# Optimization experiments

Measured on AMD Instinct MI355X. Metric: run time of the kernel, lower is better.

## Reference

```python
import jax, jax.numpy as jnp
import numpy as np

B, C, H, W = 128, 256, 32, 32
TD, NHEADS, PH, PW = 192, 4, 4, 4
FF = 384
MAXG = 8
TABLE = (2 * MAXG - 1) ** 2  # 225


def setup_inputs() -> dict:
    key = jax.random.key(0)
    ks = jax.random.split(key, 10)
    rn = lambda k, shape, s=0.02: jax.random.normal(k, shape, jnp.float32) * s
    return {
        "x": jax.random.normal(ks[0], (B, C, H, W), jnp.float32),
        "conv1_w": rn(ks[1], (TD, C)),          # 1x1 conv, no bias
        "conv2_w": rn(ks[2], (C, TD)),          # 1x1 conv, no bias
        "qkv_w": rn(ks[3], (TD, 3 * TD)), "qkv_b": jnp.zeros((3 * TD,), jnp.float32),
        "proj_w": rn(ks[4], (TD, TD)), "proj_b": jnp.zeros((TD,), jnp.float32),
        "ffn_w1": rn(ks[5], (TD, FF)), "ffn_b1": jnp.zeros((FF,), jnp.float32),
        "ffn_w2": rn(ks[6], (FF, TD)), "ffn_b2": jnp.zeros((TD,), jnp.float32),
        "ln1_g": jnp.ones((TD,), jnp.float32), "ln1_b": jnp.zeros((TD,), jnp.float32),
        "ln2_g": jnp.ones((TD,), jnp.float32), "ln2_b": jnp.zeros((TD,), jnp.float32),
        "alpha": rn(ks[7], (1,), 0.1),
        "rpb_table": rn(ks[8], (TABLE, NHEADS)),
    }


def _ln(x, g, b, eps=1e-5):
    m = x.mean(-1, keepdims=True)
    v = ((x - m) ** 2).mean(-1, keepdims=True)
    return (x - m) * jax.lax.rsqrt(v + eps) * g + b


def _rpb_index(Nh, Nw, maxg):
    # static (trace-time) relative position index over the patch grid
    ch, cw = np.meshgrid(np.arange(Nh), np.arange(Nw), indexing="ij")
    coords = np.stack([ch.ravel(), cw.ravel()])                 # (2, N)
    rel = coords[:, :, None] - coords[:, None, :]               # (2, N, N)
    idx = (rel[0] + maxg - 1) * (2 * maxg - 1) + (rel[1] + maxg - 1)
    return jnp.asarray(idx.reshape(-1), jnp.int32)              # (N*N,)


def reference(x, conv1_w, conv2_w, qkv_w, qkv_b, proj_w, proj_b,
              ffn_w1, ffn_b1, ffn_w2, ffn_b2,
              ln1_g, ln1_b, ln2_g, ln2_b, alpha, rpb_table):
    Nh, Nw = H // PH, W // PW
    Np = Nh * Nw
    hd = TD // NHEADS
    scale = 1.0 / np.sqrt(hd).astype(np.float32)

    # local 1x1 conv
    xl = jnp.einsum("bchw,tc->bthw", x, conv1_w)                # (B, TD, H, W)
    # patchify + mean-pool -> one token per patch
    xp = xl.reshape(B, TD, Nh, PH, Nw, PW).transpose(0, 2, 4, 3, 5, 1)
    xp = xp.reshape(B, Np, PH * PW, TD)
    tokens = xp.mean(axis=2)                                    # (B, Np, TD)

    # attention with gathered relative position bias
    t = _ln(tokens, ln1_g, ln1_b)
    qkv = (t @ qkv_w + qkv_b).reshape(B, Np, 3, NHEADS, hd)
    q, k, v = qkv[:, :, 0], qkv[:, :, 1], qkv[:, :, 2]          # (B, Np, H, hd)
    attn = jnp.einsum("bnhd,bmhd->bhnm", q, k) * scale
    bias = rpb_table[_rpb_index(Nh, Nw, MAXG)]                  # (Np*Np, heads)
    bias = bias.reshape(Np, Np, NHEADS).transpose(2, 0, 1)      # (heads, Np, Np)
    attn = jax.nn.softmax(attn + bias[None], axis=-1)
    o = jnp.einsum("bhnm,bmhd->bnhd", attn, v).reshape(B, Np, TD)
    o = o @ proj_w + proj_b

    out = tokens + alpha * o                                    # scaled residual
    h2 = _ln(out, ln2_g, ln2_b)
    out = out + (jax.nn.gelu(h2 @ ffn_w1 + ffn_b1, approximate=False) @ ffn_w2 + ffn_b2)

    # unpatchify: broadcast each token back over its ph*pw pixels
    ot = jnp.broadcast_to(out[:, :, None, :], (B, Np, PH * PW, TD))
    ot = ot.reshape(B, Nh, Nw, PH, PW, TD).transpose(0, 5, 1, 3, 2, 4)
    ot = ot.reshape(B, TD, H, W)
    return x + jnp.einsum("bthw,ct->bchw", ot, conv2_w)
```

## Files before the change

kernel.cpp:

```cpp
#include <hip/hip_runtime.h>
#include <hip/hip_bf16.h>

#define Bsz 128
#define Cch 256
#define Him 32
#define Wim 32
#define TD 192
#define NH 4
#define HD 48
#define FF 384
#define NP 64

typedef float f32x4 __attribute__((ext_vector_type(4)));
typedef __bf16 bf16x8 __attribute__((ext_vector_type(8)));
typedef unsigned int u32;

#define MFMA(a, b, c) __builtin_amdgcn_mfma_f32_16x16x32_bf16(a, b, c, 0, 0, 0)
#define LD8(p) (*reinterpret_cast<const bf16x8*>(p))
#define VM0 asm volatile("s_waitcnt vmcnt(0)" ::: "memory")
#define VM2 asm volatile("s_waitcnt vmcnt(2)" ::: "memory")
#define VMB do { if (wlow) { asm volatile("s_waitcnt vmcnt(4)" ::: "memory"); } \
                 else      { asm volatile("s_waitcnt vmcnt(2)" ::: "memory"); } } while (0)
#define LGKM0 asm volatile("s_waitcnt lgkmcnt(0)" ::: "memory")
#define SBAR __builtin_amdgcn_s_barrier()

__device__ __forceinline__ ushort f2bf(float f) {
    union { __hip_bfloat16 h; ushort u; } cv;
    cv.h = __float2bfloat16(f);
    return cv.u;
}

__device__ __forceinline__ void gload16(const void* g, void* l) {
    __builtin_amdgcn_global_load_lds((const __attribute__((address_space(1))) u32*)g,
                                     (__attribute__((address_space(3))) u32*)l, 16, 0, 0);
}

template <int K2B>
__device__ __forceinline__ void stageW(char* lbuf, const char* g0, int colStrB, int tid) {
    constexpr int CHB = 32 * K2B;
    constexpr int NR = (CHB + 8191) / 8192;
#pragma unroll
    for (int rd = 0; rd < NR; ++rd) {
        int p = rd * 8192 + tid * 16;
        if (p < CHB) {
            int col = p / K2B;
            int kb = (p - col * K2B) ^ ((col & 7) << 4);
            gload16(g0 + (size_t)col * colStrB + kb, lbuf + p);
        }
    }
}

typedef ushort ushort8v __attribute__((ext_vector_type(8)));
__global__ __launch_bounds__(256) void prep_kernel(const float* __restrict__ x,
                                                   const float* __restrict__ c1,
                                                   const float* __restrict__ c2,
                                                   const float* __restrict__ qw,
                                                   const float* __restrict__ pw,
                                                   const float* __restrict__ f1,
                                                   const float* __restrict__ f2,
                                                   ushort* __restrict__ wb,
                                                   ushort* __restrict__ xm) {
    const int bb = blockIdx.x;
    const int tid = threadIdx.x;
    if (bb < 1536) {
        int g = bb * 256 + tid;
        float v;
        if (g < 49152) v = c1[g];
        else if (g < 98304) v = c2[g - 49152];
        else if (g < 208896) { int i = g - 98304;  int n = i / 192, k = i - n * 192; v = qw[k * 576 + n]; }
        else if (g < 245760) { int i = g - 208896; int n = i / 192, k = i - n * 192; v = pw[k * 192 + n]; }
        else if (g < 319488) { int i = g - 245760; int n = i / 192, k = i - n * 192; v = f1[k * 384 + n]; }
        else                 { int i = g - 319488; int n = i / 384, k = i - n * 384; v = f2[k * 192 + n]; }
        wb[g] = f2bf(v);
        return;
    }
    __shared__ float acc[32][65];
    int pb = bb - 1536;
    int b = pb >> 3, cg = pb & 7;
    int c = tid >> 3, wq = tid & 7;
    const float* pl = x + ((size_t)(b * Cch + cg * 32 + c) * 1024) + wq * 4;
#pragma unroll 1
    for (int nh = 0; nh < 8; ++nh) {
        const float* p0 = pl + nh * 128;
        float4 v0 = *reinterpret_cast<const float4*>(p0);
        float4 v1 = *reinterpret_cast<const float4*>(p0 + 32);
        float4 v2 = *reinterpret_cast<const float4*>(p0 + 64);
        float4 v3 = *reinterpret_cast<const float4*>(p0 + 96);
        float s = v0.x + v0.y + v0.z + v0.w + v1.x + v1.y + v1.z + v1.w +
                  v2.x + v2.y + v2.z + v2.w + v3.x + v3.y + v3.z + v3.w;
        acc[c][nh * 8 + wq] = s * 0.0625f;
    }
    __syncthreads();
    int p = tid >> 2, c8 = (tid & 3) * 8;
    ushort8v o;
#pragma unroll
    for (int k = 0; k < 8; ++k) o[k] = f2bf(acc[c8 + k][p]);
    *reinterpret_cast<ushort8v*>(xm + ((size_t)(b * 64 + p)) * 256 + cg * 32 + c8) = o;
}

__global__ __launch_bounds__(512, 1) void token_kernel(
    const ushort* __restrict__ xm, const ushort* __restrict__ wb,
    const float* __restrict__ qkv_b, const float* __restrict__ proj_b,
    const float* __restrict__ ffn_b1, const float* __restrict__ ffn_b2,
    const float* __restrict__ ln1_g, const float* __restrict__ ln1_b,
    const float* __restrict__ ln2_g, const float* __restrict__ ln2_b,
    const float* __restrict__ alphap, const float* __restrict__ rpb,
    ushort* __restrict__ y) {
    __shared__ __align__(16) char LDS[154624];
    ushort* tln = (ushort*)(LDS);
    ushort* qb  = (ushort*)(LDS + 25600);
    ushort* kb  = (ushort*)(LDS + 51200);
    ushort* vT  = (ushort*)(LDS + 76800);
    char*   SBB = LDS + 104448;
    float2* scr2 = (float2*)(LDS + 153600);
    ushort* t2  = tln;
    ushort* obp = qb;
    ushort* h0  = qb;
    ushort* h1  = kb;
    ushort* o2  = vT;
#define SBUF(i) (SBB + (i) * 12288)

    const int b = blockIdx.x;
    const int tid = threadIdx.x, lane = tid & 63, w = tid >> 6;
    const int l15 = lane & 15, slot = lane >> 4, slot16 = slot * 16;
    const int r = w >> 1, cc = w & 1;
    const int rowA = r * 16 + l15;
    const int orow = r * 16 + slot * 4;
    const int xp = (l15 & 7) << 4;
    const int colB = cc * 16 + l15;
    const bool wlow = (w < 4);

    float qbr[18], f1br[12], l1gr[6], l1br[6], l2gr[6], l2br[6], pbr[6], f2br[6];
#pragma unroll
    for (int j = 0; j < 18; ++j) qbr[j] = qkv_b[(j / 6) * 192 + (j % 6) * 32 + colB];
#pragma unroll
    for (int j = 0; j < 12; ++j) f1br[j] = ffn_b1[j * 32 + colB];
#pragma unroll
    for (int c = 0; c < 6; ++c) {
        int col = c * 32 + colB;
        l1gr[c] = ln1_g[col]; l1br[c] = ln1_b[col];
        l2gr[c] = ln2_g[col]; l2br[c] = ln2_b[col];
        pbr[c] = proj_b[col]; f2br[c] = ffn_b2[col];
    }
    const float alpha = alphap[0];

    const char* xrow = (const char*)xm + ((size_t)(b * 64 + rowA)) * 512;
    bf16x8 a1[2][4];
#pragma unroll
    for (int kh = 0; kh < 2; ++kh)
#pragma unroll
        for (int ks = 0; ks < 4; ++ks)
            a1[kh][ks] = LD8(xrow + kh * 256 + ks * 64 + slot16);

    const char* c1g = (const char*)wb;
    const char* qg  = (const char*)(wb + 98304);
    const char* pg  = (const char*)(wb + 208896);
    const char* fg  = (const char*)(wb + 245760);
    const char* f2g = (const char*)(wb + 319488);
    const char* c2g = (const char*)(wb + 49152);

    f32x4 tok[6], pj[6];
#pragma unroll
    for (int c = 0; c < 6; ++c) { tok[c] = f32x4{0,0,0,0}; pj[c] = f32x4{0,0,0,0}; }

    stageW<256>(SBUF(0), c1g, 512, tid);
    stageW<256>(SBUF(1), c1g + 256, 512, tid);
    stageW<256>(SBUF(2), c1g + 16384, 512, tid);
#pragma unroll
    for (int j = 0; j < 12; ++j) {
        if (j < 10) VM2; else VM0;
        SBAR;
        if (j < 9) {
            int jn = j + 3;
            stageW<256>(SBUF(jn & 3), c1g + (size_t)(jn >> 1) * 16384 + (jn & 1) * 256, 512, tid);
        }
        const char* bp = SBUF(j & 3) + colB * 256;
        int c = j >> 1, kh = j & 1;
#pragma unroll
        for (int ks = 0; ks < 4; ++ks)
            tok[c] = MFMA(a1[kh][ks], LD8(bp + ((ks * 64 + slot16) ^ xp)), tok[c]);
    }
    stageW<384>(SBUF(0), qg, 384, tid);
    stageW<384>(SBUF(1), qg + 12288, 384, tid);
    stageW<384>(SBUF(2), qg + 24576, 384, tid);
    {
        float s[4] = {}, s2[4] = {};
#pragma unroll
        for (int c = 0; c < 6; ++c)
#pragma unroll
            for (int j2 = 0; j2 < 4; ++j2) { float v = tok[c][j2]; s[j2] += v; s2[j2] += v * v; }
#pragma unroll
        for (int m = 1; m < 16; m <<= 1)
#pragma unroll
            for (int j2 = 0; j2 < 4; ++j2) { s[j2] += __shfl_xor(s[j2], m); s2[j2] += __shfl_xor(s2[j2], m); }
        if (l15 == 0)
#pragma unroll
            for (int j2 = 0; j2 < 4; ++j2) scr2[(orow + j2) * 2 + cc] = make_float2(s[j2], s2[j2]);
        LGKM0; SBAR;
#pragma unroll
        for (int j2 = 0; j2 < 4; ++j2) {
            int row = orow + j2;
            float2 eA = scr2[row * 2], eB = scr2[row * 2 + 1];
            float mean = (eA.x + eB.x) * (1.f / 192.f);
            float inv = rsqrtf((eA.y + eB.y) * (1.f / 192.f) - mean * mean + 1e-5f);
#pragma unroll
            for (int c = 0; c < 6; ++c)
                tln[row * 200 + c * 32 + colB] = f2bf((tok[c][j2] - mean) * inv * l1gr[c] + l1br[c]);
        }
        LGKM0; SBAR;
    }

    {
        bf16x8 aT[6];
        const char* trow = (const char*)tln + rowA * 400;
#pragma unroll
        for (int ks = 0; ks < 6; ++ks) aT[ks] = LD8(trow + ks * 64 + slot16);
#pragma unroll
        for (int j = 0; j < 18; ++j) {
            if (j < 16) VMB; else VM0;
            SBAR;
            if (j < 15) stageW<384>(SBUF((j + 3) & 3), qg + (size_t)(j + 3) * 12288, 384, tid);
            const char* bp = SBUF(j & 3) + colB * 384;
            f32x4 acc = f32x4{0,0,0,0};
#pragma unroll
            for (int ks = 0; ks < 6; ++ks)
                acc = MFMA(aT[ks], LD8(bp + ((ks * 64 + slot16) ^ xp)), acc);
            int col = (j % 6) * 32 + colB;
            float bias = qbr[j];
            if (j < 6) {
#pragma unroll
                for (int j2 = 0; j2 < 4; ++j2) qb[(orow + j2) * 200 + col] = f2bf(acc[j2] + bias);
            } else if (j < 12) {
#pragma unroll
                for (int j2 = 0; j2 < 4; ++j2) kb[(orow + j2) * 200 + col] = f2bf(acc[j2] + bias);
            } else {
                ushort4 pk;
                pk.x = f2bf(acc[0] + bias); pk.y = f2bf(acc[1] + bias);
                pk.z = f2bf(acc[2] + bias); pk.w = f2bf(acc[3] + bias);
                *reinterpret_cast<ushort4*>(&vT[col * 72 + orow]) = pk;
            }
        }
    }
    LGKM0; SBAR;

    {
        const float scale = 0.14433756729740643f;
        ushort* P2b0 = (ushort*)(LDS + cc * 9216);
        ushort* P2b1 = (ushort*)(LDS + 104448 + cc * 9216);
#pragma unroll
        for (int p = 0; p < 2; ++p) {
            int h = p * 2 + cc;
            ushort* P2 = p ? P2b1 : P2b0;
            float rb[4][4];
#pragma unroll
            for (int j2 = 0; j2 < 4; ++j2) {
                int qrow = orow + j2, qh = qrow >> 3, qw = qrow & 7;
#pragma unroll
                for (int nf = 0; nf < 4; ++nf) {
                    int krow = l15 + nf * 16;
                    rb[j2][nf] = rpb[((qh - (krow >> 3) + 7) * 15 + (qw - (krow & 7) + 7)) * 4 + h];
                }
            }
            uint4 z = make_uint4(0, 0, 0, 0);
            const char* qrp = (const char*)qb + rowA * 400 + h * 96;
            uint4 qa1 = *(const uint4*)(qrp + slot16);
            uint4 qa2 = (slot < 2) ? *(const uint4*)(qrp + 64 + slot16) : z;
            f32x4 S[4] = {};
#pragma unroll
            for (int nf = 0; nf < 4; ++nf) {
                const char* kp = (const char*)kb + (l15 + nf * 16) * 400 + h * 96;
                uint4 k1 = *(const uint4*)(kp + slot16);
                uint4 k2 = (slot < 2) ? *(const uint4*)(kp + 64 + slot16) : z;
                S[nf] = MFMA(*(bf16x8*)&qa1, *(bf16x8*)&k1, S[nf]);
                S[nf] = MFMA(*(bf16x8*)&qa2, *(bf16x8*)&k2, S[nf]);
            }
#pragma unroll
            for (int j2 = 0; j2 < 4; ++j2) {
                float sv[4]; float mx = -1e30f;
#pragma unroll
                for (int nf = 0; nf < 4; ++nf) { sv[nf] = S[nf][j2] * scale + rb[j2][nf]; mx = fmaxf(mx, sv[nf]); }
#pragma unroll
                for (int m = 1; m < 16; m <<= 1) mx = fmaxf(mx, __shfl_xor(mx, m));
                float sum = 0.f;
#pragma unroll
                for (int nf = 0; nf < 4; ++nf) { sv[nf] = expf(sv[nf] - mx); sum += sv[nf]; }
#pragma unroll
                for (int m = 1; m < 16; m <<= 1) sum += __shfl_xor(sum, m);
                float inv = 1.f / sum;
                int qrow = orow + j2;
#pragma unroll
                for (int nf = 0; nf < 4; ++nf) P2[qrow * 72 + l15 + nf * 16] = f2bf(sv[nf] * inv);
            }
        }
        LGKM0; SBAR;
#pragma unroll
        for (int p = 0; p < 2; ++p) {
            int h = p * 2 + cc;
            ushort* P2 = p ? P2b1 : P2b0;
            f32x4 O[3] = {};
            const char* prow = (const char*)P2 + rowA * 144;
#pragma unroll
            for (int ki = 0; ki < 2; ++ki) {
                bf16x8 pa = LD8(prow + ki * 64 + slot16);
#pragma unroll
                for (int nf = 0; nf < 3; ++nf) {
                    bf16x8 vb = LD8((const char*)vT + (h * 48 + l15 + nf * 16) * 144 + ki * 64 + slot16);
                    O[nf] = MFMA(pa, vb, O[nf]);
                }
            }
#pragma unroll
            for (int nf = 0; nf < 3; ++nf)
#pragma unroll
                for (int j2 = 0; j2 < 4; ++j2)
                    obp[(orow + j2) * 200 + h * 48 + l15 + nf * 16] = f2bf(O[nf][j2]);
        }
        LGKM0; SBAR;
    }
    stageW<384>(SBUF(0), pg, 384, tid);
    stageW<384>(SBUF(1), pg + 12288, 384, tid);
    stageW<384>(SBUF(2), pg + 24576, 384, tid);

    {
        bf16x8 aO[6];
        const char* orw = (const char*)obp + rowA * 400;
#pragma unroll
        for (int ks = 0; ks < 6; ++ks) aO[ks] = LD8(orw + ks * 64 + slot16);
#pragma unroll
        for (int j = 0; j < 6; ++j) {
            if (j < 4) VMB; else VM0;
            SBAR;
            if (j < 3) stageW<384>(SBUF((j + 3) & 3), pg + (size_t)(j + 3) * 12288, 384, tid);
            const char* bp = SBUF(j & 3) + colB * 384;
#pragma unroll
            for (int ks = 0; ks < 6; ++ks)
                pj[j] = MFMA(aO[ks], LD8(bp + ((ks * 64 + slot16) ^ xp)), pj[j]);
        }
    }
    SBAR;
    stageW<384>(SBUF(0), fg, 384, tid);
    stageW<384>(SBUF(1), fg + 12288, 384, tid);
    stageW<384>(SBUF(2), fg + 24576, 384, tid);
    {
        float s[4] = {}, s2[4] = {};
#pragma unroll
        for (int c = 0; c < 6; ++c)
#pragma unroll
            for (int j2 = 0; j2 < 4; ++j2) {
                float v = tok[c][j2] + alpha * (pj[c][j2] + pbr[c]);
                pj[c][j2] = v;
                s[j2] += v; s2[j2] += v * v;
            }
#pragma unroll
        for (int m = 1; m < 16; m <<= 1)
#pragma unroll
            for (int j2 = 0; j2 < 4; ++j2) { s[j2] += __shfl_xor(s[j2], m); s2[j2] += __shfl_xor(s2[j2], m); }
        if (l15 == 0)
#pragma unroll
            for (int j2 = 0; j2 < 4; ++j2) scr2[(orow + j2) * 2 + cc] = make_float2(s[j2], s2[j2]);
        LGKM0; SBAR;
#pragma unroll
        for (int j2 = 0; j2 < 4; ++j2) {
            int row = orow + j2;
            float2 eA = scr2[row * 2], eB = scr2[row * 2 + 1];
            float mean = (eA.x + eB.x) * (1.f / 192.f);
            float inv = rsqrtf((eA.y + eB.y) * (1.f / 192.f) - mean * mean + 1e-5f);
#pragma unroll
            for (int c = 0; c < 6; ++c)
                t2[row * 200 + c * 32 + colB] = f2bf((pj[c][j2] - mean) * inv * l2gr[c] + l2br[c]);
        }
        LGKM0; SBAR;
    }

    {
        bf16x8 aT2[6];
        const char* trow = (const char*)t2 + rowA * 400;
#pragma unroll
        for (int ks = 0; ks < 6; ++ks) aT2[ks] = LD8(trow + ks * 64 + slot16);
#pragma unroll
        for (int j = 0; j < 12; ++j) {
            if (j < 10) VMB; else VM0;
            SBAR;
            if (j < 9) stageW<384>(SBUF((j + 3) & 3), fg + (size_t)(j + 3) * 12288, 384, tid);
            const char* bp = SBUF(j & 3) + colB * 384;
            f32x4 acc = f32x4{0,0,0,0};
#pragma unroll
            for (int ks = 0; ks < 6; ++ks)
                acc = MFMA(aT2[ks], LD8(bp + ((ks * 64 + slot16) ^ xp)), acc);
            int col384 = j * 32 + colB;
            ushort* hb = (j < 6) ? h0 : h1;
            int lcol = (j < 6) ? col384 : col384 - 192;
#pragma unroll
            for (int j2 = 0; j2 < 4; ++j2) {
                float v = acc[j2] + f1br[j];
                v = 0.5f * v * (1.f + erff(v * 0.70710678118654752f));
                hb[(orow + j2) * 200 + lcol] = f2bf(v);
            }
        }
    }
    LGKM0; SBAR;
    stageW<384>(SBUF(0), f2g, 768, tid);
    stageW<384>(SBUF(1), f2g + 384, 768, tid);
    stageW<384>(SBUF(2), f2g + 24576, 768, tid);

    f32x4 f2a[6];
#pragma unroll
    for (int c = 0; c < 6; ++c) f2a[c] = f32x4{0,0,0,0};
    {
        bf16x8 ah[2][6];
        const char* h0r = (const char*)h0 + rowA * 400;
        const char* h1r = (const char*)h1 + rowA * 400;
#pragma unroll
        for (int ks = 0; ks < 6; ++ks) {
            ah[0][ks] = LD8(h0r + ks * 64 + slot16);
            ah[1][ks] = LD8(h1r + ks * 64 + slot16);
        }
#pragma unroll
        for (int j = 0; j < 12; ++j) {
            if (j < 10) VMB; else VM0;
            SBAR;
            if (j < 9) {
                int jn = j + 3;
                stageW<384>(SBUF(jn & 3), f2g + (size_t)(jn >> 1) * 24576 + (jn & 1) * 384, 768, tid);
            }
            const char* bp = SBUF(j & 3) + colB * 384;
            int c = j >> 1, kh = j & 1;
#pragma unroll
            for (int ks = 0; ks < 6; ++ks)
                f2a[c] = MFMA(ah[kh][ks], LD8(bp + ((ks * 64 + slot16) ^ xp)), f2a[c]);
        }
    }
    stageW<384>(SBUF(0), c2g, 384, tid);
    stageW<384>(SBUF(1), c2g + 12288, 384, tid);
    stageW<384>(SBUF(2), c2g + 24576, 384, tid);
#pragma unroll
    for (int c = 0; c < 6; ++c) {
        int col = c * 32 + colB;
#pragma unroll
        for (int j2 = 0; j2 < 4; ++j2)
            o2[(orow + j2) * 200 + col] = f2bf(pj[c][j2] + f2a[c][j2] + f2br[c]);
    }
    LGKM0; SBAR;

    {
        bf16x8 aO2[6];
        const char* o2r = (const char*)o2 + rowA * 400;
#pragma unroll
        for (int ks = 0; ks < 6; ++ks) aO2[ks] = LD8(o2r + ks * 64 + slot16);
        ushort* yb = y + (size_t)b * 64 * 256;
#pragma unroll
        for (int j = 0; j < 8; ++j) {
            if (j < 6) VMB; else VM0;
            SBAR;
            if (j < 5) stageW<384>(SBUF((j + 3) & 3), c2g + (size_t)(j + 3) * 12288, 384, tid);
            const char* bp = SBUF(j & 3) + colB * 384;
            f32x4 acc = f32x4{0,0,0,0};
#pragma unroll
            for (int ks = 0; ks < 6; ++ks)
                acc = MFMA(aO2[ks], LD8(bp + ((ks * 64 + slot16) ^ xp)), acc);
            int col = j * 32 + colB;
#pragma unroll
            for (int j2 = 0; j2 < 4; ++j2)
                yb[(size_t)(orow + j2) * 256 + col] = f2bf(acc[j2]);
        }
    }
#undef SBUF
}

__global__ __launch_bounds__(256) void final_kernel(const float* __restrict__ x,
                                                    const ushort* __restrict__ y,
                                                    float* __restrict__ out) {
    size_t g = (size_t)blockIdx.x * 256 + threadIdx.x;
    int w4 = g & 7, hh = (g >> 3) & 31, c = (g >> 8) & 255, b = (int)(g >> 16);
    int p = (hh >> 2) * 8 + w4;
    u32 yu = y[((size_t)b * NP + p) * Cch + c];
    union { u32 u; float f; } cv; cv.u = yu << 16;
    float yv = cv.f;
    f32x4 xv = *(reinterpret_cast<const f32x4*>(x) + g);
    f32x4 ov = {xv.x + yv, xv.y + yv, xv.z + yv, xv.w + yv};
    __builtin_nontemporal_store(ov, reinterpret_cast<f32x4*>(out) + g);
}

extern "C" void kernel_launch(void* const* d_in, const int* in_sizes, int n_in,
                              void* d_out, int out_size, void* d_ws, size_t ws_size,
                              hipStream_t stream) {
    const float* x       = (const float*)d_in[0];
    const float* conv1_w = (const float*)d_in[1];
    const float* conv2_w = (const float*)d_in[2];
    const float* qkv_w   = (const float*)d_in[3];
    const float* qkv_b   = (const float*)d_in[4];
    const float* proj_w  = (const float*)d_in[5];
    const float* proj_b  = (const float*)d_in[6];
    const float* ffn_w1  = (const float*)d_in[7];
    const float* ffn_b1  = (const float*)d_in[8];
    const float* ffn_w2  = (const float*)d_in[9];
    const float* ffn_b2  = (const float*)d_in[10];
    const float* ln1_g   = (const float*)d_in[11];
    const float* ln1_b   = (const float*)d_in[12];
    const float* ln2_g   = (const float*)d_in[13];
    const float* ln2_b   = (const float*)d_in[14];
    const float* alpha   = (const float*)d_in[15];
    const float* rpb     = (const float*)d_in[16];
    float* out = (float*)d_out;

    ushort* ybuf = (ushort*)d_ws;
    ushort* xm   = ybuf + 2097152;
    ushort* wb   = xm + 2097152;

    prep_kernel<<<2560, 256, 0, stream>>>(x, conv1_w, conv2_w, qkv_w, proj_w, ffn_w1, ffn_w2,
                                          wb, xm);
    token_kernel<<<Bsz, 512, 0, stream>>>(xm, wb, qkv_b, proj_b, ffn_b1, ffn_b2,
                                          ln1_g, ln1_b, ln2_g, ln2_b, alpha, rpb, ybuf);
    final_kernel<<<(Bsz * Cch * Him * Wim) / 1024, 256, 0, stream>>>(x, ybuf, out);
}
```

Before: 111.2 us.

## Double token kernel workgroup to 1024 threads, split column tiles across wave pairs

The token kernel now runs 16 waves per batch instead of 8. Each GEMM stage processes two weight column tiles at once, one per wave half, with double staging per barrier. Attention now gives each wave one head instead of looping over two. The 3-deep prefetch pipeline with partial vmcnt waits becomes a full wait plus barrier each step, so more waves hide latency but the overlap of loads with MFMA may shrink. Biases are moved into LDS or loaded per use instead of being held in registers.

```diff
diff --git a/kernel.cpp b/kernel.cpp
--- a/kernel.cpp
+++ b/kernel.cpp
@@ -14,13 +14,11 @@
 typedef float f32x4 __attribute__((ext_vector_type(4)));
 typedef __bf16 bf16x8 __attribute__((ext_vector_type(8)));
 typedef unsigned int u32;
+typedef ushort ushort8v __attribute__((ext_vector_type(8)));
 
 #define MFMA(a, b, c) __builtin_amdgcn_mfma_f32_16x16x32_bf16(a, b, c, 0, 0, 0)
 #define LD8(p) (*reinterpret_cast<const bf16x8*>(p))
 #define VM0 asm volatile("s_waitcnt vmcnt(0)" ::: "memory")
-#define VM2 asm volatile("s_waitcnt vmcnt(2)" ::: "memory")
-#define VMB do { if (wlow) { asm volatile("s_waitcnt vmcnt(4)" ::: "memory"); } \
-                 else      { asm volatile("s_waitcnt vmcnt(2)" ::: "memory"); } } while (0)
 #define LGKM0 asm volatile("s_waitcnt lgkmcnt(0)" ::: "memory")
 #define SBAR __builtin_amdgcn_s_barrier()
 
@@ -38,19 +36,14 @@
 template <int K2B>
 __device__ __forceinline__ void stageW(char* lbuf, const char* g0, int colStrB, int tid) {
     constexpr int CHB = 32 * K2B;
-    constexpr int NR = (CHB + 8191) / 8192;
-#pragma unroll
-    for (int rd = 0; rd < NR; ++rd) {
-        int p = rd * 8192 + tid * 16;
-        if (p < CHB) {
-            int col = p / K2B;
-            int kb = (p - col * K2B) ^ ((col & 7) << 4);
-            gload16(g0 + (size_t)col * colStrB + kb, lbuf + p);
-        }
-    }
-}
-
-typedef ushort ushort8v __attribute__((ext_vector_type(8)));
+    int p = tid * 16;
+    if (p < CHB) {
+        int col = p / K2B;
+        int kb = (p - col * K2B) ^ ((col & 7) << 4);
+        gload16(g0 + (size_t)col * colStrB + kb, lbuf + p);
+    }
+}
+
 __global__ __launch_bounds__(256) void prep_kernel(const float* __restrict__ x,
                                                    const float* __restrict__ c1,
                                                    const float* __restrict__ c2,
@@ -98,7 +91,7 @@
     *reinterpret_cast<ushort8v*>(xm + ((size_t)(b * 64 + p)) * 256 + cg * 32 + c8) = o;
 }
 
-__global__ __launch_bounds__(512, 1) void token_kernel(
+__global__ __launch_bounds__(1024, 1) void token_kernel(
     const ushort* __restrict__ xm, const ushort* __restrict__ wb,
     const float* __restrict__ qkv_b, const float* __restrict__ proj_b,
     const float* __restrict__ ffn_b1, const float* __restrict__ ffn_b2,
@@ -106,13 +99,16 @@
     const float* __restrict__ ln2_g, const float* __restrict__ ln2_b,
     const float* __restrict__ alphap, const float* __restrict__ rpb,
     ushort* __restrict__ y) {
-    __shared__ __align__(16) char LDS[154624];
+    __shared__ __align__(16) char LDS[160000];
     ushort* tln = (ushort*)(LDS);
     ushort* qb  = (ushort*)(LDS + 25600);
     ushort* kb  = (ushort*)(LDS + 51200);
     ushort* vT  = (ushort*)(LDS + 76800);
     char*   SBB = LDS + 104448;
-    float2* scr2 = (float2*)(LDS + 153600);
+    float2* scrP = (float2*)(LDS + 153600);
+    float2* scrS = (float2*)(LDS + 155648);
+    float*  qbl  = (float*)(LDS + 156160);
+    float*  f1bl = (float*)(LDS + 158464);
     ushort* t2  = tln;
     ushort* obp = qb;
     ushort* h0  = qb;
@@ -123,34 +119,14 @@
     const int b = blockIdx.x;
     const int tid = threadIdx.x, lane = tid & 63, w = tid >> 6;
     const int l15 = lane & 15, slot = lane >> 4, slot16 = slot * 16;
-    const int r = w >> 1, cc = w & 1;
+    const int r = w & 3, h4 = (w >> 2) & 3, p = w >> 3;
     const int rowA = r * 16 + l15;
     const int orow = r * 16 + slot * 4;
     const int xp = (l15 & 7) << 4;
-    const int colB = cc * 16 + l15;
-    const bool wlow = (w < 4);
-
-    float qbr[18], f1br[12], l1gr[6], l1br[6], l2gr[6], l2br[6], pbr[6], f2br[6];
-#pragma unroll
-    for (int j = 0; j < 18; ++j) qbr[j] = qkv_b[(j / 6) * 192 + (j % 6) * 32 + colB];
-#pragma unroll
-    for (int j = 0; j < 12; ++j) f1br[j] = ffn_b1[j * 32 + colB];
-#pragma unroll
-    for (int c = 0; c < 6; ++c) {
-        int col = c * 32 + colB;
-        l1gr[c] = ln1_g[col]; l1br[c] = ln1_b[col];
-        l2gr[c] = ln2_g[col]; l2br[c] = ln2_b[col];
-        pbr[c] = proj_b[col]; f2br[c] = ffn_b2[col];
-    }
-    const float alpha = alphap[0];
-
-    const char* xrow = (const char*)xm + ((size_t)(b * 64 + rowA)) * 512;
-    bf16x8 a1[2][4];
-#pragma unroll
-    for (int kh = 0; kh < 2; ++kh)
-#pragma unroll
-        for (int ks = 0; ks < 4; ++ks)
-            a1[kh][ks] = LD8(xrow + kh * 256 + ks * 64 + slot16);
+    const int colB = ((w >> 2) & 1) * 16 + l15;
+
+    if (tid < 576) qbl[tid] = qkv_b[tid];
+    if (tid < 384) f1bl[tid] = ffn_b1[tid];
 
     const char* c1g = (const char*)wb;
     const char* qg  = (const char*)(wb + 98304);
@@ -159,85 +135,103 @@
     const char* f2g = (const char*)(wb + 319488);
     const char* c2g = (const char*)(wb + 49152);
 
-    f32x4 tok[6], pj[6];
-#pragma unroll
-    for (int c = 0; c < 6; ++c) { tok[c] = f32x4{0,0,0,0}; pj[c] = f32x4{0,0,0,0}; }
-
-    stageW<256>(SBUF(0), c1g, 512, tid);
-    stageW<256>(SBUF(1), c1g + 256, 512, tid);
-    stageW<256>(SBUF(2), c1g + 16384, 512, tid);
-#pragma unroll
-    for (int j = 0; j < 12; ++j) {
-        if (j < 10) VM2; else VM0;
-        SBAR;
-        if (j < 9) {
-            int jn = j + 3;
-            stageW<256>(SBUF(jn & 3), c1g + (size_t)(jn >> 1) * 16384 + (jn & 1) * 256, 512, tid);
-        }
+    bf16x8 a1[2][4];
+#pragma unroll
+    for (int kh = 0; kh < 2; ++kh)
+#pragma unroll
+        for (int ks = 0; ks < 4; ++ks)
+            a1[kh][ks] = LD8(xm + (size_t)(b * 64 + rowA) * 256 + kh * 128 + ks * 32 + slot * 8);
+
+    f32x4 tok[3] = {}, pj[3] = {}, f2a[3] = {};
+
+    stageW<256>(SBUF(0), c1g + (size_t)0 * 16384, 512, tid);
+    stageW<256>(SBUF(1), c1g + (size_t)1 * 16384, 512, tid);
+#pragma unroll
+    for (int s = 0; s < 6; ++s) {
+        VM0; SBAR;
+        if (s < 5) {
+            int ja = 2 * s + 2, jb = 2 * s + 3;
+            stageW<256>(SBUF(ja & 3), c1g + (size_t)(ja % 6) * 16384 + (ja / 6) * 256, 512, tid);
+            stageW<256>(SBUF(jb & 3), c1g + (size_t)(jb % 6) * 16384 + (jb / 6) * 256, 512, tid);
+        }
+        int j = 2 * s + p;
         const char* bp = SBUF(j & 3) + colB * 256;
-        int c = j >> 1, kh = j & 1;
+        const int kh = s / 3, li = s % 3;
 #pragma unroll
         for (int ks = 0; ks < 4; ++ks)
-            tok[c] = MFMA(a1[kh][ks], LD8(bp + ((ks * 64 + slot16) ^ xp)), tok[c]);
+            tok[li] = MFMA(a1[kh][ks], LD8(bp + ((ks * 64 + slot16) ^ xp)), tok[li]);
     }
     stageW<384>(SBUF(0), qg, 384, tid);
     stageW<384>(SBUF(1), qg + 12288, 384, tid);
-    stageW<384>(SBUF(2), qg + 24576, 384, tid);
-    {
-        float s[4] = {}, s2[4] = {};
-#pragma unroll
-        for (int c = 0; c < 6; ++c)
-#pragma unroll
-            for (int j2 = 0; j2 < 4; ++j2) { float v = tok[c][j2]; s[j2] += v; s2[j2] += v * v; }
+
+    {
+        float s1v[4] = {}, s2v[4] = {};
+#pragma unroll
+        for (int i = 0; i < 3; ++i)
+#pragma unroll
+            for (int j2 = 0; j2 < 4; ++j2) { float v = tok[i][j2]; s1v[j2] += v; s2v[j2] += v * v; }
 #pragma unroll
         for (int m = 1; m < 16; m <<= 1)
 #pragma unroll
-            for (int j2 = 0; j2 < 4; ++j2) { s[j2] += __shfl_xor(s[j2], m); s2[j2] += __shfl_xor(s2[j2], m); }
+            for (int j2 = 0; j2 < 4; ++j2) { s1v[j2] += __shfl_xor(s1v[j2], m); s2v[j2] += __shfl_xor(s2v[j2], m); }
         if (l15 == 0)
 #pragma unroll
-            for (int j2 = 0; j2 < 4; ++j2) scr2[(orow + j2) * 2 + cc] = make_float2(s[j2], s2[j2]);
+            for (int j2 = 0; j2 < 4; ++j2) scrP[(orow + j2) * 4 + h4] = make_float2(s1v[j2], s2v[j2]);
         LGKM0; SBAR;
-#pragma unroll
-        for (int j2 = 0; j2 < 4; ++j2) {
-            int row = orow + j2;
-            float2 eA = scr2[row * 2], eB = scr2[row * 2 + 1];
-            float mean = (eA.x + eB.x) * (1.f / 192.f);
-            float inv = rsqrtf((eA.y + eB.y) * (1.f / 192.f) - mean * mean + 1e-5f);
-#pragma unroll
-            for (int c = 0; c < 6; ++c)
-                tln[row * 200 + c * 32 + colB] = f2bf((tok[c][j2] - mean) * inv * l1gr[c] + l1br[c]);
+        {
+            float sx = 0.f, sy = 0.f;
+#pragma unroll
+            for (int g2 = 0; g2 < 4; ++g2) { float2 e = scrP[lane * 4 + g2]; sx += e.x; sy += e.y; }
+            float mean = sx * (1.f / 192.f);
+            float inv = rsqrtf(sy * (1.f / 192.f) - mean * mean + 1e-5f);
+            scrS[lane] = make_float2(mean, inv);
+        }
+        LGKM0;
+#pragma unroll
+        for (int i = 0; i < 3; ++i) {
+            int col = (2 * i + p) * 32 + colB;
+            float gg = ln1_g[col], bb2 = ln1_b[col];
+#pragma unroll
+            for (int j2 = 0; j2 < 4; ++j2) {
+                int row = orow + j2;
+                float2 st = scrS[row];
+                tln[row * 200 + col] = f2bf((tok[i][j2] - st.x) * st.y * gg + bb2);
+            }
         }
         LGKM0; SBAR;
     }
 
     {
         bf16x8 aT[6];
-        const char* trow = (const char*)tln + rowA * 400;
-#pragma unroll
-        for (int ks = 0; ks < 6; ++ks) aT[ks] = LD8(trow + ks * 64 + slot16);
-#pragma unroll
-        for (int j = 0; j < 18; ++j) {
-            if (j < 16) VMB; else VM0;
-            SBAR;
-            if (j < 15) stageW<384>(SBUF((j + 3) & 3), qg + (size_t)(j + 3) * 12288, 384, tid);
+#pragma unroll
+        for (int ks = 0; ks < 6; ++ks) aT[ks] = LD8((const char*)tln + rowA * 400 + ks * 64 + slot16);
+#pragma unroll
+        for (int s = 0; s < 9; ++s) {
+            VM0; SBAR;
+            if (s < 8) {
+                stageW<384>(SBUF((2 * s + 2) & 3), qg + (size_t)(2 * s + 2) * 12288, 384, tid);
+                stageW<384>(SBUF((2 * s + 3) & 3), qg + (size_t)(2 * s + 3) * 12288, 384, tid);
+            }
+            int j = 2 * s + p;
             const char* bp = SBUF(j & 3) + colB * 384;
-            f32x4 acc = f32x4{0,0,0,0};
+            f32x4 acc = f32x4{0, 0, 0, 0};
 #pragma unroll
             for (int ks = 0; ks < 6; ++ks)
                 acc = MFMA(aT[ks], LD8(bp + ((ks * 64 + slot16) ^ xp)), acc);
-            int col = (j % 6) * 32 + colB;
-            float bias = qbr[j];
-            if (j < 6) {
-#pragma unroll
-                for (int j2 = 0; j2 < 4; ++j2) qb[(orow + j2) * 200 + col] = f2bf(acc[j2] + bias);
-            } else if (j < 12) {
-#pragma unroll
-                for (int j2 = 0; j2 < 4; ++j2) kb[(orow + j2) * 200 + col] = f2bf(acc[j2] + bias);
+            const int sel = s / 3;
+            int colj = (j - sel * 6) * 32 + colB;
+            float bias = qbl[sel * 192 + colj];
+            if (sel == 0) {
+#pragma unroll
+                for (int j2 = 0; j2 < 4; ++j2) qb[(orow + j2) * 200 + colj] = f2bf(acc[j2] + bias);
+            } else if (sel == 1) {
+#pragma unroll
+                for (int j2 = 0; j2 < 4; ++j2) kb[(orow + j2) * 200 + colj] = f2bf(acc[j2] + bias);
             } else {
                 ushort4 pk;
                 pk.x = f2bf(acc[0] + bias); pk.y = f2bf(acc[1] + bias);
                 pk.z = f2bf(acc[2] + bias); pk.w = f2bf(acc[3] + bias);
-                *reinterpret_cast<ushort4*>(&vT[col * 72 + orow]) = pk;
+                *reinterpret_cast<ushort4*>(&vT[colj * 72 + orow]) = pk;
             }
         }
     }
@@ -245,153 +239,159 @@
 
     {
         const float scale = 0.14433756729740643f;
-        ushort* P2b0 = (ushort*)(LDS + cc * 9216);
-        ushort* P2b1 = (ushort*)(LDS + 104448 + cc * 9216);
-#pragma unroll
-        for (int p = 0; p < 2; ++p) {
-            int h = p * 2 + cc;
-            ushort* P2 = p ? P2b1 : P2b0;
-            float rb[4][4];
-#pragma unroll
-            for (int j2 = 0; j2 < 4; ++j2) {
-                int qrow = orow + j2, qh = qrow >> 3, qw = qrow & 7;
-#pragma unroll
-                for (int nf = 0; nf < 4; ++nf) {
-                    int krow = l15 + nf * 16;
-                    rb[j2][nf] = rpb[((qh - (krow >> 3) + 7) * 15 + (qw - (krow & 7) + 7)) * 4 + h];
-                }
-            }
-            uint4 z = make_uint4(0, 0, 0, 0);
-            const char* qrp = (const char*)qb + rowA * 400 + h * 96;
-            uint4 qa1 = *(const uint4*)(qrp + slot16);
-            uint4 qa2 = (slot < 2) ? *(const uint4*)(qrp + 64 + slot16) : z;
-            f32x4 S[4] = {};
+        ushort* P2 = (ushort*)(LDS + 104448 + h4 * 9216);
+        float rb[4][4];
+#pragma unroll
+        for (int j2 = 0; j2 < 4; ++j2) {
+            int qrow = orow + j2, qh = qrow >> 3, qw = qrow & 7;
 #pragma unroll
             for (int nf = 0; nf < 4; ++nf) {
-                const char* kp = (const char*)kb + (l15 + nf * 16) * 400 + h * 96;
-                uint4 k1 = *(const uint4*)(kp + slot16);
-                uint4 k2 = (slot < 2) ? *(const uint4*)(kp + 64 + slot16) : z;
-                S[nf] = MFMA(*(bf16x8*)&qa1, *(bf16x8*)&k1, S[nf]);
-                S[nf] = MFMA(*(bf16x8*)&qa2, *(bf16x8*)&k2, S[nf]);
-            }
-#pragma unroll
-            for (int j2 = 0; j2 < 4; ++j2) {
-                float sv[4]; float mx = -1e30f;
-#pragma unroll
-                for (int nf = 0; nf < 4; ++nf) { sv[nf] = S[nf][j2] * scale + rb[j2][nf]; mx = fmaxf(mx, sv[nf]); }
-#pragma unroll
-                for (int m = 1; m < 16; m <<= 1) mx = fmaxf(mx, __shfl_xor(mx, m));
-                float sum = 0.f;
-#pragma unroll
-                for (int nf = 0; nf < 4; ++nf) { sv[nf] = expf(sv[nf] - mx); sum += sv[nf]; }
-#pragma unroll
-                for (int m = 1; m < 16; m <<= 1) sum += __shfl_xor(sum, m);
-                float inv = 1.f / sum;
-                int qrow = orow + j2;
-#pragma unroll
-                for (int nf = 0; nf < 4; ++nf) P2[qrow * 72 + l15 + nf * 16] = f2bf(sv[nf] * inv);
-            }
+                int krow = l15 + nf * 16;
+                rb[j2][nf] = rpb[((qh - (krow >> 3) + 7) * 15 + (qw - (krow & 7) + 7)) * 4 + h4];
+            }
+        }
+        uint4 z = make_uint4(0, 0, 0, 0);
+        const char* qrp = (const char*)qb + rowA * 400 + h4 * 96;
+        uint4 qa1 = *(const uint4*)(qrp + slot16);
+        uint4 qa2 = (slot < 2) ? *(const uint4*)(qrp + 64 + slot16) : z;
+        f32x4 S[4] = {};
+#pragma unroll
+        for (int nf = 0; nf < 4; ++nf) {
+            const char* kp = (const char*)kb + (l15 + nf * 16) * 400 + h4 * 96;
+            uint4 k1 = *(const uint4*)(kp + slot16);
+            uint4 k2 = (slot < 2) ? *(const uint4*)(kp + 64 + slot16) : z;
+            S[nf] = MFMA(*(bf16x8*)&qa1, *(bf16x8*)&k1, S[nf]);
+            S[nf] = MFMA(*(bf16x8*)&qa2, *(bf16x8*)&k2, S[nf]);
+        }
+#pragma unroll
+        for (int j2 = 0; j2 < 4; ++j2) {
+            float sv[4]; float mx = -1e30f;
+#pragma unroll
+            for (int nf = 0; nf < 4; ++nf) { sv[nf] = S[nf][j2] * scale + rb[j2][nf]; mx = fmaxf(mx, sv[nf]); }
+#pragma unroll
+            for (int m = 1; m < 16; m <<= 1) mx = fmaxf(mx, __shfl_xor(mx, m));
+            float sum = 0.f;
+#pragma unroll
+            for (int nf = 0; nf < 4; ++nf) { sv[nf] = expf(sv[nf] - mx); sum += sv[nf]; }
+#pragma unroll
+            for (int m = 1; m < 16; m <<= 1) sum += __shfl_xor(sum, m);
+            float inv = 1.f / sum;
+            int qrow = orow + j2;
+#pragma unroll
+            for (int nf = 0; nf < 4; ++nf) P2[qrow * 72 + l15 + nf * 16] = f2bf(sv[nf] * inv);
         }
         LGKM0; SBAR;
-#pragma unroll
-        for (int p = 0; p < 2; ++p) {
-            int h = p * 2 + cc;
-            ushort* P2 = p ? P2b1 : P2b0;
-            f32x4 O[3] = {};
-            const char* prow = (const char*)P2 + rowA * 144;
-#pragma unroll
-            for (int ki = 0; ki < 2; ++ki) {
-                bf16x8 pa = LD8(prow + ki * 64 + slot16);
-#pragma unroll
-                for (int nf = 0; nf < 3; ++nf) {
-                    bf16x8 vb = LD8((const char*)vT + (h * 48 + l15 + nf * 16) * 144 + ki * 64 + slot16);
-                    O[nf] = MFMA(pa, vb, O[nf]);
-                }
-            }
-#pragma unroll
-            for (int nf = 0; nf < 3; ++nf)
-#pragma unroll
-                for (int j2 = 0; j2 < 4; ++j2)
-                    obp[(orow + j2) * 200 + h * 48 + l15 + nf * 16] = f2bf(O[nf][j2]);
-        }
+        f32x4 O[3] = {};
+        const char* prow = (const char*)P2 + rowA * 144;
+#pragma unroll
+        for (int ki = 0; ki < 2; ++ki) {
+            bf16x8 pa = LD8(prow + ki * 64 + slot16);
+#pragma unroll
+            for (int nf = 0; nf < 3; ++nf) {
+                bf16x8 vb = LD8((const char*)vT + (h4 * 48 + l15 + nf * 16) * 144 + ki * 64 + slot16);
+                O[nf] = MFMA(pa, vb, O[nf]);
+            }
+        }
+#pragma unroll
+        for (int nf = 0; nf < 3; ++nf)
+#pragma unroll
+            for (int j2 = 0; j2 < 4; ++j2)
+                obp[(orow + j2) * 200 + h4 * 48 + l15 + nf * 16] = f2bf(O[nf][j2]);
         LGKM0; SBAR;
     }
     stageW<384>(SBUF(0), pg, 384, tid);
     stageW<384>(SBUF(1), pg + 12288, 384, tid);
-    stageW<384>(SBUF(2), pg + 24576, 384, tid);
 
     {
         bf16x8 aO[6];
-        const char* orw = (const char*)obp + rowA * 400;
-#pragma unroll
-        for (int ks = 0; ks < 6; ++ks) aO[ks] = LD8(orw + ks * 64 + slot16);
-#pragma unroll
-        for (int j = 0; j < 6; ++j) {
-            if (j < 4) VMB; else VM0;
-            SBAR;
-            if (j < 3) stageW<384>(SBUF((j + 3) & 3), pg + (size_t)(j + 3) * 12288, 384, tid);
+#pragma unroll
+        for (int ks = 0; ks < 6; ++ks) aO[ks] = LD8((const char*)obp + rowA * 400 + ks * 64 + slot16);
+#pragma unroll
+        for (int s = 0; s < 3; ++s) {
+            VM0; SBAR;
+            if (s < 2) {
+                stageW<384>(SBUF((2 * s + 2) & 3), pg + (size_t)(2 * s + 2) * 12288, 384, tid);
+                stageW<384>(SBUF((2 * s + 3) & 3), pg + (size_t)(2 * s + 3) * 12288, 384, tid);
+            }
+            int j = 2 * s + p;
             const char* bp = SBUF(j & 3) + colB * 384;
+            f32x4 acc = f32x4{0, 0, 0, 0};
 #pragma unroll
             for (int ks = 0; ks < 6; ++ks)
-                pj[j] = MFMA(aO[ks], LD8(bp + ((ks * 64 + slot16) ^ xp)), pj[j]);
-        }
-    }
-    SBAR;
-    stageW<384>(SBUF(0), fg, 384, tid);
-    stageW<384>(SBUF(1), fg + 12288, 384, tid);
-    stageW<384>(SBUF(2), fg + 24576, 384, tid);
-    {
-        float s[4] = {}, s2[4] = {};
-#pragma unroll
-        for (int c = 0; c < 6; ++c)
+                acc = MFMA(aO[ks], LD8(bp + ((ks * 64 + slot16) ^ xp)), acc);
+            pj[s] = acc;
+        }
+    }
+    {
+        const float alpha = alphap[0];
+        float s1v[4] = {}, s2v[4] = {};
+#pragma unroll
+        for (int i = 0; i < 3; ++i) {
+            int col = (2 * i + p) * 32 + colB;
+            float pb = proj_b[col];
 #pragma unroll
             for (int j2 = 0; j2 < 4; ++j2) {
-                float v = tok[c][j2] + alpha * (pj[c][j2] + pbr[c]);
-                pj[c][j2] = v;
-                s[j2] += v; s2[j2] += v * v;
-            }
+                float v = tok[i][j2] + alpha * (pj[i][j2] + pb);
+                pj[i][j2] = v;
+                s1v[j2] += v; s2v[j2] += v * v;
+            }
+        }
 #pragma unroll
         for (int m = 1; m < 16; m <<= 1)
 #pragma unroll
-            for (int j2 = 0; j2 < 4; ++j2) { s[j2] += __shfl_xor(s[j2], m); s2[j2] += __shfl_xor(s2[j2], m); }
+            for (int j2 = 0; j2 < 4; ++j2) { s1v[j2] += __shfl_xor(s1v[j2], m); s2v[j2] += __shfl_xor(s2v[j2], m); }
         if (l15 == 0)
 #pragma unroll
-            for (int j2 = 0; j2 < 4; ++j2) scr2[(orow + j2) * 2 + cc] = make_float2(s[j2], s2[j2]);
+            for (int j2 = 0; j2 < 4; ++j2) scrP[(orow + j2) * 4 + h4] = make_float2(s1v[j2], s2v[j2]);
         LGKM0; SBAR;
-#pragma unroll
-        for (int j2 = 0; j2 < 4; ++j2) {
-            int row = orow + j2;
-            float2 eA = scr2[row * 2], eB = scr2[row * 2 + 1];
-            float mean = (eA.x + eB.x) * (1.f / 192.f);
-            float inv = rsqrtf((eA.y + eB.y) * (1.f / 192.f) - mean * mean + 1e-5f);
-#pragma unroll
-            for (int c = 0; c < 6; ++c)
-                t2[row * 200 + c * 32 + colB] = f2bf((pj[c][j2] - mean) * inv * l2gr[c] + l2br[c]);
+        stageW<384>(SBUF(0), fg, 384, tid);
+        stageW<384>(SBUF(1), fg + 12288, 384, tid);
+        {
+            float sx = 0.f, sy = 0.f;
+#pragma unroll
+            for (int g2 = 0; g2 < 4; ++g2) { float2 e = scrP[lane * 4 + g2]; sx += e.x; sy += e.y; }
+            float mean = sx * (1.f / 192.f);
+            float inv = rsqrtf(sy * (1.f / 192.f) - mean * mean + 1e-5f);
+            scrS[lane] = make_float2(mean, inv);
+        }
+        LGKM0;
+#pragma unroll
+        for (int i = 0; i < 3; ++i) {
+            int col = (2 * i + p) * 32 + colB;
+            float gg = ln2_g[col], bb2 = ln2_b[col];
+#pragma unroll
+            for (int j2 = 0; j2 < 4; ++j2) {
+                int row = orow + j2;
+                float2 st = scrS[row];
+                t2[row * 200 + col] = f2bf((pj[i][j2] - st.x) * st.y * gg + bb2);
+            }
         }
         LGKM0; SBAR;
     }
 
     {
         bf16x8 aT2[6];
-        const char* trow = (const char*)t2 + rowA * 400;
-#pragma unroll
-        for (int ks = 0; ks < 6; ++ks) aT2[ks] = LD8(trow + ks * 64 + slot16);
-#pragma unroll
-        for (int j = 0; j < 12; ++j) {
-            if (j < 10) VMB; else VM0;
-            SBAR;
-            if (j < 9) stageW<384>(SBUF((j + 3) & 3), fg + (size_t)(j + 3) * 12288, 384, tid);
+#pragma unroll
+        for (int ks = 0; ks < 6; ++ks) aT2[ks] = LD8((const char*)t2 + rowA * 400 + ks * 64 + slot16);
+#pragma unroll
+        for (int s = 0; s < 6; ++s) {
+            VM0; SBAR;
+            if (s < 5) {
+                stageW<384>(SBUF((2 * s + 2) & 3), fg + (size_t)(2 * s + 2) * 12288, 384, tid);
+                stageW<384>(SBUF((2 * s + 3) & 3), fg + (size_t)(2 * s + 3) * 12288, 384, tid);
+            }
+            int j = 2 * s + p;
             const char* bp = SBUF(j & 3) + colB * 384;
-            f32x4 acc = f32x4{0,0,0,0};
+            f32x4 acc = f32x4{0, 0, 0, 0};
 #pragma unroll
             for (int ks = 0; ks < 6; ++ks)
                 acc = MFMA(aT2[ks], LD8(bp + ((ks * 64 + slot16) ^ xp)), acc);
-            int col384 = j * 32 + colB;
-            ushort* hb = (j < 6) ? h0 : h1;
-            int lcol = (j < 6) ? col384 : col384 - 192;
+            ushort* hb = (s < 3) ? h0 : h1;
+            int lcol = (j - (s < 3 ? 0 : 6)) * 32 + colB;
+            float bias = f1bl[j * 32 + colB];
 #pragma unroll
             for (int j2 = 0; j2 < 4; ++j2) {
-                float v = acc[j2] + f1br[j];
+                float v = acc[j2] + bias;
                 v = 0.5f * v * (1.f + erff(v * 0.70710678118654752f));
                 hb[(orow + j2) * 200 + lcol] = f2bf(v);
             }
@@ -399,61 +399,60 @@
     }
     LGKM0; SBAR;
     stageW<384>(SBUF(0), f2g, 768, tid);
-    stageW<384>(SBUF(1), f2g + 384, 768, tid);
-    stageW<384>(SBUF(2), f2g + 24576, 768, tid);
-
-    f32x4 f2a[6];
-#pragma unroll
-    for (int c = 0; c < 6; ++c) f2a[c] = f32x4{0,0,0,0};
-    {
-        bf16x8 ah[2][6];
-        const char* h0r = (const char*)h0 + rowA * 400;
-        const char* h1r = (const char*)h1 + rowA * 400;
+    stageW<384>(SBUF(1), f2g + 24576, 768, tid);
+
+    {
+        bf16x8 ah0[6], ah1[6];
 #pragma unroll
         for (int ks = 0; ks < 6; ++ks) {
-            ah[0][ks] = LD8(h0r + ks * 64 + slot16);
-            ah[1][ks] = LD8(h1r + ks * 64 + slot16);
-        }
-#pragma unroll
-        for (int j = 0; j < 12; ++j) {
-            if (j < 10) VMB; else VM0;
-            SBAR;
-            if (j < 9) {
-                int jn = j + 3;
-                stageW<384>(SBUF(jn & 3), f2g + (size_t)(jn >> 1) * 24576 + (jn & 1) * 384, 768, tid);
-            }
+            ah0[ks] = LD8((const char*)h0 + rowA * 400 + ks * 64 + slot16);
+            ah1[ks] = LD8((const char*)h1 + rowA * 400 + ks * 64 + slot16);
+        }
+#pragma unroll
+        for (int s = 0; s < 6; ++s) {
+            VM0; SBAR;
+            if (s < 5) {
+                int ja = 2 * s + 2, jb = 2 * s + 3;
+                stageW<384>(SBUF(ja & 3), f2g + (size_t)(ja % 6) * 24576 + (ja / 6) * 384, 768, tid);
+                stageW<384>(SBUF(jb & 3), f2g + (size_t)(jb % 6) * 24576 + (jb / 6) * 384, 768, tid);
+            }
+            int j = 2 * s + p;
             const char* bp = SBUF(j & 3) + colB * 384;
-            int c = j >> 1, kh = j & 1;
-#pragma unroll
-            for (int ks = 0; ks < 6; ++ks)
-                f2a[c] = MFMA(ah[kh][ks], LD8(bp + ((ks * 64 + slot16) ^ xp)), f2a[c]);
+            const int kh = s / 3, li = s % 3;
+#pragma unroll
+            for (int ks = 0; ks < 6; ++ks) {
+                bf16x8 af = kh ? ah1[ks] : ah0[ks];
+                f2a[li] = MFMA(af, LD8(bp + ((ks * 64 + slot16) ^ xp)), f2a[li]);
+            }
         }
     }
     stageW<384>(SBUF(0), c2g, 384, tid);
     stageW<384>(SBUF(1), c2g + 12288, 384, tid);
-    stageW<384>(SBUF(2), c2g + 24576, 384, tid);
-#pragma unroll
-    for (int c = 0; c < 6; ++c) {
-        int col = c * 32 + colB;
+#pragma unroll
+    for (int i = 0; i < 3; ++i) {
+        int col = (2 * i + p) * 32 + colB;
+        float fb = ffn_b2[col];
 #pragma unroll
         for (int j2 = 0; j2 < 4; ++j2)
-            o2[(orow + j2) * 200 + col] = f2bf(pj[c][j2] + f2a[c][j2] + f2br[c]);
+            o2[(orow + j2) * 200 + col] = f2bf(pj[i][j2] + f2a[i][j2] + fb);
     }
     LGKM0; SBAR;
 
     {
         bf16x8 aO2[6];
-        const char* o2r = (const char*)o2 + rowA * 400;
-#pragma unroll
-        for (int ks = 0; ks < 6; ++ks) aO2[ks] = LD8(o2r + ks * 64 + slot16);
+#pragma unroll
+        for (int ks = 0; ks < 6; ++ks) aO2[ks] = LD8((const char*)o2 + rowA * 400 + ks * 64 + slot16);
         ushort* yb = y + (size_t)b * 64 * 256;
 #pragma unroll
-        for (int j = 0; j < 8; ++j) {
-            if (j < 6) VMB; else VM0;
-            SBAR;
-            if (j < 5) stageW<384>(SBUF((j + 3) & 3), c2g + (size_t)(j + 3) * 12288, 384, tid);
+        for (int s = 0; s < 4; ++s) {
+            VM0; SBAR;
+            if (s < 3) {
+                stageW<384>(SBUF((2 * s + 2) & 3), c2g + (size_t)(2 * s + 2) * 12288, 384, tid);
+                stageW<384>(SBUF((2 * s + 3) & 3), c2g + (size_t)(2 * s + 3) * 12288, 384, tid);
+            }
+            int j = 2 * s + p;
             const char* bp = SBUF(j & 3) + colB * 384;
-            f32x4 acc = f32x4{0,0,0,0};
+            f32x4 acc = f32x4{0, 0, 0, 0};
 #pragma unroll
             for (int ks = 0; ks < 6; ++ks)
                 acc = MFMA(aO2[ks], LD8(bp + ((ks * 64 + slot16) ^ xp)), acc);
@@ -508,7 +507,7 @@
 
     prep_kernel<<<2560, 256, 0, stream>>>(x, conv1_w, conv2_w, qkv_w, proj_w, ffn_w1, ffn_w2,
                                           wb, xm);
-    token_kernel<<<Bsz, 512, 0, stream>>>(xm, wb, qkv_b, proj_b, ffn_b1, ffn_b2,
-                                          ln1_g, ln1_b, ln2_g, ln2_b, alpha, rpb, ybuf);
+    token_kernel<<<Bsz, 1024, 0, stream>>>(xm, wb, qkv_b, proj_b, ffn_b1, ffn_b2,
+                                           ln1_g, ln1_b, ln2_g, ln2_b, alpha, rpb, ybuf);
     final_kernel<<<(Bsz * Cch * Him * Wim) / 1024, 256, 0, stream>>>(x, ybuf, out);
 }
```

New measurement: 114.4 us. 1.03x slower.
